# Optimization experiments

Measured on AMD Instinct MI355X. Metric: run time of the kernel, lower is better.

The kernel has to match this reference:

```python
import jax, jax.numpy as jnp
import numpy as np

# gen_dx_bx([-30,30,0.15], [-15,15,0.15])
DX = jnp.array([0.15, 0.15], dtype=jnp.float32)
BX = jnp.array([-29.925, -14.925], dtype=jnp.float32)


def _pairwise_dist(a, b):
    # torch.cdist p=2: [Na,2] x [Nb,2] -> [Na,Nb]
    return jnp.sqrt(jnp.sum((a[:, None, :] - b[None, :, :]) ** 2, axis=-1))


def _single(match, position, semantic, pts, ins, typ):
    # match [M,M] (M=N+1 with dustbin), position [N,2], semantic [C,N],
    # pts [G,2], ins [G] int, typ [G] int. Assumes mask is all-ones (set in setup_inputs).
    N = position.shape[0]
    M = match.shape[0]
    G = pts.shape[0]
    C = semantic.shape[0]

    pos = position * DX + BX                      # grid -> meters
    cd = _pairwise_dist(pos, pts)                 # [N,G]
    nearest = cd.argmin(-1).astype(jnp.int32)     # [N]
    cdist_mean = jnp.mean(cd.min(-1))             # mean of per-pred nearest-GT distance
    dist_map = _pairwise_dist(pos, pos)           # [N,N]
    nmax = nearest.max()

    # precompute, for every gt index g, whether any pred maps to it and the
    # closest such pred (torch: idx_pred_next[cdist[idx_pred_next, g].argmin()])
    assign = nearest[:, None] == jnp.arange(G, dtype=jnp.int32)[None, :]  # [N,G]
    exists_g = assign.any(0)                                              # [G]
    best_pred_g = jnp.where(assign, cd, jnp.inf).argmin(0).astype(jnp.int32)  # [G]

    def walk(start_gt):
        # greedy forward walk along gt indices; replicates the python while-loop,
        # including torch's negative-index wrap (idx % G) for idx_gt_next = -1.
        def cond(st):
            return ~st[2]

        def body(st):
            idx, steps, done, res = st
            is_end = idx >= nmax
            g_next_raw = jnp.where(is_end, jnp.int32(-1), idx + 1)
            g_next = jnp.mod(g_next_raw, G)
            ex = (~is_end) & exists_g[g_next]  # nearest==-1 never holds in torch
            same = ins[jnp.mod(idx, G)] == ins[g_next]
            matched = ex & same
            stop = matched | (~same) | (steps >= G + 2)  # safety bound
            res_new = jnp.where(matched, best_pred_g[g_next], jnp.int32(-1))
            return (g_next_raw, steps + jnp.int32(1), stop, res_new)

        st = (start_gt, jnp.int32(0), jnp.bool_(False), jnp.int32(-1))
        return jax.lax.while_loop(cond, body, st)[3]

    next_pred = jax.vmap(walk)(nearest)  # [N], -1 means no match (dustbin later)

    # build match_gt [M,M]
    A = jnp.zeros((M, M), dtype=match.dtype)
    valid = next_pred >= 0
    cols = jnp.where(valid, next_pred, 0)
    A = A.at[jnp.arange(N), cols].max(valid.astype(match.dtype))

    # resolve columns matched by multiple rows: keep the row closest in dist_map
    Acols = A[:, :N]
    col_sum = Acols.sum(0)
    dist_pad = jnp.concatenate([dist_map, jnp.full((1, N), jnp.inf, dist_map.dtype)], 0)  # [M,N]
    keep = jnp.where(Acols > 0, dist_pad, jnp.inf).argmin(0)  # [N]
    onehot = (jnp.arange(M)[:, None] == keep[None, :]).astype(match.dtype)
    Acols = jnp.where(col_sum[None, :] > 1, onehot, Acols)
    A = A.at[:, :N].set(Acols)

    # unmatched pred rows -> dustbin column; unmatched pred cols -> dustbin row
    row_sum = A[:N].sum(1)
    A = A.at[:N, M - 1].set(jnp.where(row_sum == 0, 1.0, A[:N, M - 1]))
    col_sum2 = A[:, :N].sum(0)
    A = A.at[M - 1, :N].set(jnp.where(col_sum2 == 0, 1.0, A[M - 1, :N]))

    # semantic gt: one-hot of the type of each pred's nearest gt point
    cls = typ[nearest]  # [N]
    semantic_gt = (jnp.arange(C)[:, None] == cls[None, :]).astype(semantic.dtype)  # [C,N]

    # NLL match loss (torch transposes then feeds NLLLoss: loss = -match[j, target[j]])
    tgt_b = A.argmax(0)  # per-column gt row
    tgt_f = A.argmax(1)  # per-row gt col
    j = jnp.arange(M - 1)
    loss_b = -jnp.mean(match[j, tgt_b[: M - 1]])
    loss_f = -jnp.mean(match[j, tgt_f[: M - 1]])
    match_loss = 0.5 * (loss_f + loss_b)

    sem_loss = -jnp.mean(semantic[semantic_gt.argmax(0), jnp.arange(N)])
    return cdist_mean, match_loss, sem_loss, A, semantic_gt


def setup_inputs() -> dict:
    key = jax.random.key(0)
    ks = jax.random.split(key, 5)
    B, N, G, C, NI = 4, 2048, 1024, 3, 32
    # log-probability score matrix with dustbin (Sinkhorn-style output)
    matches = jax.nn.log_softmax(jax.random.normal(ks[0], (B, N + 1, N + 1), jnp.float32), axis=-1)
    # predicted vertex grid coords on the 400x200 BEV grid
    positions = jax.random.uniform(ks[1], (B, N, 2), jnp.float32) * jnp.array([400.0, 200.0], jnp.float32)
    semantics = jax.nn.log_softmax(jax.random.normal(ks[2], (B, C, N), jnp.float32), axis=1)
    masks = jnp.ones((B, N, 1), jnp.float32)
    # gt points in meters within the BEV range
    gt_pts = (jax.random.uniform(ks[3], (B, G, 2), jnp.float32) - 0.5) * jnp.array([60.0, 30.0], jnp.float32)
    # sorted instance ids -> contiguous runs like the original per-instance list build
    gt_ins = jnp.sort(jax.random.randint(ks[4], (B, G), 0, NI), axis=-1).astype(jnp.int32)
    gt_type = (gt_ins % C).astype(jnp.int32)
    return {"matches": matches, "positions": positions, "semantics": semantics,
            "masks": masks, "gt_pts": gt_pts, "gt_ins": gt_ins, "gt_type": gt_type}


def reference(matches, positions, semantics, masks, gt_pts, gt_ins, gt_type):
    cm, ml, sl, mg, sg = jax.vmap(_single)(matches, positions, semantics, gt_pts, gt_ins, gt_type)
    # reduction='mean'
    return jnp.mean(cm), jnp.mean(ml), jnp.mean(sl), mg, sg
```

## Files before the change

### kernel.cpp

```cpp
#include <hip/hip_runtime.h>
#include <math.h>

#define BB 4
#define NN 2048
#define GG 1024
#define CC 3
#define MM 2049
#define SP 8
#define CH (GG / SP)

typedef unsigned long long u64;
#define KEY_EMPTY 0xFFFFFFFFFFFFFFFFULL

struct Ws {
  u64   near_key[BB * NN];
  u64   best_key[BB * GG];
  u64   keep_key[BB * NN];
  int   nearest[BB * NN];
  int   next_pred[BB * NN];
  int   col_cnt[BB * NN];
  int   nmax[BB];
  float cdist_sum[BB];
  float sem_sum[BB];
  float lossf_sum[BB];
  float lossb_sum[BB];
};

__device__ __forceinline__ float posx(float p) { return __fadd_rn(__fmul_rn(p, 0.15f), -29.925f); }
__device__ __forceinline__ float posy(float p) { return __fadd_rn(__fmul_rn(p, 0.15f), -14.925f); }
__device__ __forceinline__ float pdist(float ax, float ay, float bx, float by) {
  float dx = __fsub_rn(ax, bx);
  float dy = __fsub_rn(ay, by);
  return __fsqrt_rn(__fadd_rn(__fmul_rn(dx, dx), __fmul_rn(dy, dy)));
}
__device__ __forceinline__ u64 pack_key(float d, int i) {
  return ((u64)__float_as_uint(d) << 32) | (unsigned int)i;
}


__global__ void k_init(Ws* ws) {
  int t = blockIdx.x * blockDim.x + threadIdx.x;
  if (t < BB * NN) {
    ws->near_key[t] = KEY_EMPTY;
    ws->keep_key[t] = KEY_EMPTY;
    ws->col_cnt[t] = 0;
  }
  if (t < BB * GG) ws->best_key[t] = KEY_EMPTY;
  if (t < BB) {
    ws->nmax[t] = 0;
    ws->cdist_sum[t] = 0.f;
    ws->sem_sum[t] = 0.f;
    ws->lossf_sum[t] = 0.f;
    ws->lossb_sum[t] = 0.f;
  }
}

__global__ __launch_bounds__(256) void k_near1(const float* __restrict__ positions,
                                               const float* __restrict__ gt_pts, Ws* ws) {
  __shared__ float spts[CH * 2];
  const int cpb = NN / 256;
  int b = blockIdx.x / (cpb * SP);
  int r = blockIdx.x % (cpb * SP);
  int i = (r / SP) * 256 + threadIdx.x;
  int g0 = (r % SP) * CH;

  spts[threadIdx.x] = gt_pts[b * GG * 2 + g0 * 2 + threadIdx.x];
  __syncthreads();

  float px = posx(positions[(size_t)(b * NN + i) * 2 + 0]);
  float py = posy(positions[(size_t)(b * NN + i) * 2 + 1]);

  float dmin = INFINITY;
  int gmin = 0;
  #pragma unroll 4
  for (int g = 0; g < CH; ++g) {
    float d = pdist(px, py, spts[2 * g], spts[2 * g + 1]);
    if (d < dmin) { dmin = d; gmin = g; }
  }
  atomicMin(&ws->near_key[b * NN + i], pack_key(dmin, g0 + gmin));
}

__global__ __launch_bounds__(64) void k_near2(const int* __restrict__ gt_type,
                                              const float* __restrict__ semantics,
                                              Ws* ws, float* __restrict__ out) {
  int b = blockIdx.x >> 5;
  int i = (blockIdx.x & 31) * 64 + threadIdx.x;

  u64 key = ws->near_key[b * NN + i];
  float dmin = __uint_as_float((unsigned int)(key >> 32));
  int g = (int)(key & 0xFFFFFFFFULL);

  ws->nearest[b * NN + i] = g;
  atomicMin(&ws->best_key[b * GG + g], pack_key(dmin, i));

  int cls = gt_type[b * GG + g];
  float* sg = out + 3 + (size_t)BB * MM * MM;
  sg[(size_t)b * CC * NN + 0 * NN + i] = (cls == 0) ? 1.f : 0.f;
  sg[(size_t)b * CC * NN + 1 * NN + i] = (cls == 1) ? 1.f : 0.f;
  sg[(size_t)b * CC * NN + 2 * NN + i] = (cls == 2) ? 1.f : 0.f;
  float sem = semantics[(size_t)b * CC * NN + (size_t)cls * NN + i];

  float v = dmin;
  #pragma unroll
  for (int o = 32; o > 0; o >>= 1) v += __shfl_down(v, o, 64);
  if (threadIdx.x == 0) atomicAdd(&ws->cdist_sum[b], v);

  v = sem;
  #pragma unroll
  for (int o = 32; o > 0; o >>= 1) v += __shfl_down(v, o, 64);
  if (threadIdx.x == 0) atomicAdd(&ws->sem_sum[b], v);

  int m = g;
  #pragma unroll
  for (int o = 32; o > 0; o >>= 1) m = max(m, __shfl_down(m, o, 64));
  if (threadIdx.x == 0) atomicMax(&ws->nmax[b], m);
}

__global__ __launch_bounds__(64) void k_walk(const int* __restrict__ gt_ins,
                                             const float* __restrict__ positions, Ws* ws) {
  __shared__ int sins[GG];
  __shared__ int sbest[GG];
  int b = blockIdx.x >> 5;
  int i = (blockIdx.x & 31) * 64 + threadIdx.x;

  {
    const int4* src = reinterpret_cast<const int4*>(gt_ins + b * GG);
    int4* dst = reinterpret_cast<int4*>(sins);
    for (int t = threadIdx.x; t < GG / 4; t += 64) dst[t] = src[t];
    const u64* bk = ws->best_key + b * GG;
    for (int t = threadIdx.x; t < GG; t += 64) {
      u64 k = bk[t];
      sbest[t] = (k == KEY_EMPTY) ? -1 : (int)(k & 0xFFFFFFFFULL);
    }
  }
  __syncthreads();

  int nmax = ws->nmax[b];
  int idx = ws->nearest[b * NN + i];
  int steps = 0, res = -1;
  while (true) {
    bool is_end = idx >= nmax;
    int gnr = is_end ? -1 : idx + 1;
    int gn = gnr & (GG - 1);
    bool ex = (!is_end) && (sbest[gn] >= 0);
    bool same = sins[idx & (GG - 1)] == sins[gn];
    bool matched = ex && same;
    res = matched ? sbest[gn] : -1;
    bool stop = matched || (!same) || (steps >= GG + 2);
    idx = gnr;
    ++steps;
    if (stop) break;
  }
  ws->next_pred[b * NN + i] = res;
  if (res >= 0) {
    atomicAdd(&ws->col_cnt[b * NN + res], 1);
    const float* pb = positions + (size_t)b * NN * 2;
    float d = pdist(posx(pb[2 * i]), posy(pb[2 * i + 1]),
                    posx(pb[2 * res]), posy(pb[2 * res + 1]));
    atomicMin(&ws->keep_key[b * NN + res], pack_key(d, i));
  }
}

__global__ __launch_bounds__(64) void k_post(const float* __restrict__ matches,
                                             Ws* ws, float* __restrict__ out) {
  int b = blockIdx.x >> 5;
  int i = (blockIdx.x & 31) * 64 + threadIdx.x;

  float* A = out + 3 + (size_t)b * MM * MM;

  int j = ws->next_pred[b * NN + i];
  bool surv = (j >= 0) && ((int)(ws->keep_key[b * NN + j] & 0xFFFFFFFFULL) == i);
  if (surv) A[(size_t)i * MM + j] = 1.0f;
  else      A[(size_t)i * MM + (MM - 1)] = 1.0f;

  int cnt = ws->col_cnt[b * NN + i];
  if (cnt == 0) A[(size_t)(MM - 1) * MM + i] = 1.0f;

  int tf = surv ? j : (MM - 1);
  float vf = matches[(size_t)b * MM * MM + (size_t)i * MM + tf];
  int tb = (cnt > 0) ? (int)(ws->keep_key[b * NN + i] & 0xFFFFFFFFULL) : (MM - 1);
  float vb = matches[(size_t)b * MM * MM + (size_t)i * MM + tb];

  float v = vf;
  #pragma unroll
  for (int o = 32; o > 0; o >>= 1) v += __shfl_down(v, o, 64);
  if (threadIdx.x == 0) atomicAdd(&ws->lossf_sum[b], v);

  v = vb;
  #pragma unroll
  for (int o = 32; o > 0; o >>= 1) v += __shfl_down(v, o, 64);
  if (threadIdx.x == 0) atomicAdd(&ws->lossb_sum[b], v);
}

__global__ void k_final(Ws* ws, float* __restrict__ out) {
  if (threadIdx.x == 0 && blockIdx.x == 0) {
    float cm = 0.f, ml = 0.f, sl = 0.f;
    for (int b = 0; b < BB; ++b) {
      cm += ws->cdist_sum[b] / (float)NN;
      float lf = -(ws->lossf_sum[b] / (float)(MM - 1));
      float lb = -(ws->lossb_sum[b] / (float)(MM - 1));
      ml += 0.5f * (lf + lb);
      sl += -(ws->sem_sum[b] / (float)NN);
    }
    out[0] = cm / (float)BB;
    out[1] = ml / (float)BB;
    out[2] = sl / (float)BB;
  }
}

extern "C" void kernel_launch(void* const* d_in, const int* in_sizes, int n_in,
                              void* d_out, int out_size, void* d_ws, size_t ws_size,
                              hipStream_t stream) {
  (void)in_sizes; (void)n_in; (void)ws_size;
  const float* matches   = (const float*)d_in[0];
  const float* positions = (const float*)d_in[1];
  const float* semantics = (const float*)d_in[2];
  const float* gt_pts    = (const float*)d_in[4];
  const int*   gt_ins    = (const int*)d_in[5];
  const int*   gt_type   = (const int*)d_in[6];
  float* out = (float*)d_out;
  Ws* ws = (Ws*)d_ws;

  hipMemsetAsync(d_out, 0, (size_t)out_size * sizeof(float), stream);
  k_init<<<(BB * NN + 255) / 256, 256, 0, stream>>>(ws);
  k_near1<<<BB * (NN / 256) * SP, 256, 0, stream>>>(positions, gt_pts, ws);
  k_near2<<<BB * (NN / 64), 64, 0, stream>>>(gt_type, semantics, ws, out);
  k_walk<<<BB * (NN / 64), 64, 0, stream>>>(gt_ins, positions, ws);
  k_post<<<BB * (NN / 64), 64, 0, stream>>>(matches, ws, out);
  k_final<<<1, 64, 0, stream>>>(ws, out);
}
```

Baseline: 150.8 us.

## Fuse nearest-search, walk and post kernels; fold output zeroing into kernel

Replaces the six-step launch sequence with three kernels. The nearest-GT search now splits each point's 1024 GT candidates across 8 lanes and reduces packed keys with shuffles instead of global atomics. The walk and post phases are fused into one 1024-thread block per batch that keeps counts and keep-keys in shared memory. The large output memset is replaced by a grid-stride float4 zeroing inside k_near, which removes the separate memset and init kernels. The cost is that the walk/post phase now runs on only 4 blocks, so most of the GPU sits idle during it.

```diff
diff --git a/kernel.cpp b/kernel.cpp
--- a/kernel.cpp
+++ b/kernel.cpp
@@ -6,22 +6,20 @@
 #define GG 1024
 #define CC 3
 #define MM 2049
-#define SP 8
-#define CH (GG / SP)
+#define ABEG 3
+#define ASZ (BB * MM * MM)
+#define AEND (ABEG + ASZ)
+#define A4BEG 4
+#define NF4 ((AEND - A4BEG) / 4)
 
 typedef unsigned long long u64;
 #define KEY_EMPTY 0xFFFFFFFFFFFFFFFFULL
 
 struct Ws {
-  u64   near_key[BB * NN];
   u64   best_key[BB * GG];
-  u64   keep_key[BB * NN];
   int   nearest[BB * NN];
-  int   next_pred[BB * NN];
-  int   col_cnt[BB * NN];
-  int   nmax[BB];
-  float cdist_sum[BB];
-  float sem_sum[BB];
+  float cdist_part[256];
+  float sem_part[256];
   float lossf_sum[BB];
   float lossb_sum[BB];
 };
@@ -37,170 +35,197 @@
   return ((u64)__float_as_uint(d) << 32) | (unsigned int)i;
 }
 
-
-__global__ void k_init(Ws* ws) {
-  int t = blockIdx.x * blockDim.x + threadIdx.x;
-  if (t < BB * NN) {
-    ws->near_key[t] = KEY_EMPTY;
-    ws->keep_key[t] = KEY_EMPTY;
-    ws->col_cnt[t] = 0;
-  }
-  if (t < BB * GG) ws->best_key[t] = KEY_EMPTY;
-  if (t < BB) {
-    ws->nmax[t] = 0;
-    ws->cdist_sum[t] = 0.f;
-    ws->sem_sum[t] = 0.f;
-    ws->lossf_sum[t] = 0.f;
-    ws->lossb_sum[t] = 0.f;
-  }
-}
-
-__global__ __launch_bounds__(256) void k_near1(const float* __restrict__ positions,
-                                               const float* __restrict__ gt_pts, Ws* ws) {
-  __shared__ float spts[CH * 2];
-  const int cpb = NN / 256;
-  int b = blockIdx.x / (cpb * SP);
-  int r = blockIdx.x % (cpb * SP);
-  int i = (r / SP) * 256 + threadIdx.x;
-  int g0 = (r % SP) * CH;
-
-  spts[threadIdx.x] = gt_pts[b * GG * 2 + g0 * 2 + threadIdx.x];
-  __syncthreads();
-
-  float px = posx(positions[(size_t)(b * NN + i) * 2 + 0]);
-  float py = posy(positions[(size_t)(b * NN + i) * 2 + 1]);
-
-  float dmin = INFINITY;
-  int gmin = 0;
-  #pragma unroll 4
-  for (int g = 0; g < CH; ++g) {
-    float d = pdist(px, py, spts[2 * g], spts[2 * g + 1]);
-    if (d < dmin) { dmin = d; gmin = g; }
-  }
-  atomicMin(&ws->near_key[b * NN + i], pack_key(dmin, g0 + gmin));
-}
-
-__global__ __launch_bounds__(64) void k_near2(const int* __restrict__ gt_type,
+__global__ __launch_bounds__(256) void k_near(const float* __restrict__ positions,
+                                              const float* __restrict__ gt_pts,
+                                              const int* __restrict__ gt_type,
                                               const float* __restrict__ semantics,
                                               Ws* ws, float* __restrict__ out) {
-  int b = blockIdx.x >> 5;
-  int i = (blockIdx.x & 31) * 64 + threadIdx.x;
-
-  u64 key = ws->near_key[b * NN + i];
-  float dmin = __uint_as_float((unsigned int)(key >> 32));
-  int g = (int)(key & 0xFFFFFFFFULL);
-
-  ws->nearest[b * NN + i] = g;
-  atomicMin(&ws->best_key[b * GG + g], pack_key(dmin, i));
-
-  int cls = gt_type[b * GG + g];
-  float* sg = out + 3 + (size_t)BB * MM * MM;
-  sg[(size_t)b * CC * NN + 0 * NN + i] = (cls == 0) ? 1.f : 0.f;
-  sg[(size_t)b * CC * NN + 1 * NN + i] = (cls == 1) ? 1.f : 0.f;
-  sg[(size_t)b * CC * NN + 2 * NN + i] = (cls == 2) ? 1.f : 0.f;
-  float sem = semantics[(size_t)b * CC * NN + (size_t)cls * NN + i];
-
-  float v = dmin;
-  #pragma unroll
-  for (int o = 32; o > 0; o >>= 1) v += __shfl_down(v, o, 64);
-  if (threadIdx.x == 0) atomicAdd(&ws->cdist_sum[b], v);
-
-  v = sem;
-  #pragma unroll
-  for (int o = 32; o > 0; o >>= 1) v += __shfl_down(v, o, 64);
-  if (threadIdx.x == 0) atomicAdd(&ws->sem_sum[b], v);
-
-  int m = g;
-  #pragma unroll
-  for (int o = 32; o > 0; o >>= 1) m = max(m, __shfl_down(m, o, 64));
-  if (threadIdx.x == 0) atomicMax(&ws->nmax[b], m);
-}
-
-__global__ __launch_bounds__(64) void k_walk(const int* __restrict__ gt_ins,
-                                             const float* __restrict__ positions, Ws* ws) {
-  __shared__ int sins[GG];
-  __shared__ int sbest[GG];
-  int b = blockIdx.x >> 5;
-  int i = (blockIdx.x & 31) * 64 + threadIdx.x;
+  __shared__ float spts[GG * 2];
+  __shared__ float sdm[32], ssm[32];
+  const int bid = blockIdx.x, tid = threadIdx.x;
+  const int b = bid >> 6, blk = bid & 63;
+  const int p = tid >> 3, q = tid & 7;
+  const int i = blk * 32 + p;
 
   {
-    const int4* src = reinterpret_cast<const int4*>(gt_ins + b * GG);
-    int4* dst = reinterpret_cast<int4*>(sins);
-    for (int t = threadIdx.x; t < GG / 4; t += 64) dst[t] = src[t];
-    const u64* bk = ws->best_key + b * GG;
-    for (int t = threadIdx.x; t < GG; t += 64) {
-      u64 k = bk[t];
-      sbest[t] = (k == KEY_EMPTY) ? -1 : (int)(k & 0xFFFFFFFFULL);
-    }
-  }
-  __syncthreads();
-
-  int nmax = ws->nmax[b];
-  int idx = ws->nearest[b * NN + i];
-  int steps = 0, res = -1;
-  while (true) {
-    bool is_end = idx >= nmax;
-    int gnr = is_end ? -1 : idx + 1;
-    int gn = gnr & (GG - 1);
-    bool ex = (!is_end) && (sbest[gn] >= 0);
-    bool same = sins[idx & (GG - 1)] == sins[gn];
-    bool matched = ex && same;
-    res = matched ? sbest[gn] : -1;
-    bool stop = matched || (!same) || (steps >= GG + 2);
-    idx = gnr;
-    ++steps;
-    if (stop) break;
-  }
-  ws->next_pred[b * NN + i] = res;
-  if (res >= 0) {
-    atomicAdd(&ws->col_cnt[b * NN + res], 1);
-    const float* pb = positions + (size_t)b * NN * 2;
-    float d = pdist(posx(pb[2 * i]), posy(pb[2 * i + 1]),
-                    posx(pb[2 * res]), posy(pb[2 * res + 1]));
-    atomicMin(&ws->keep_key[b * NN + res], pack_key(d, i));
-  }
-}
-
-__global__ __launch_bounds__(64) void k_post(const float* __restrict__ matches,
-                                             Ws* ws, float* __restrict__ out) {
-  int b = blockIdx.x >> 5;
-  int i = (blockIdx.x & 31) * 64 + threadIdx.x;
-
-  float* A = out + 3 + (size_t)b * MM * MM;
-
-  int j = ws->next_pred[b * NN + i];
-  bool surv = (j >= 0) && ((int)(ws->keep_key[b * NN + j] & 0xFFFFFFFFULL) == i);
-  if (surv) A[(size_t)i * MM + j] = 1.0f;
-  else      A[(size_t)i * MM + (MM - 1)] = 1.0f;
-
-  int cnt = ws->col_cnt[b * NN + i];
-  if (cnt == 0) A[(size_t)(MM - 1) * MM + i] = 1.0f;
-
-  int tf = surv ? j : (MM - 1);
-  float vf = matches[(size_t)b * MM * MM + (size_t)i * MM + tf];
-  int tb = (cnt > 0) ? (int)(ws->keep_key[b * NN + i] & 0xFFFFFFFFULL) : (MM - 1);
-  float vb = matches[(size_t)b * MM * MM + (size_t)i * MM + tb];
-
-  float v = vf;
-  #pragma unroll
-  for (int o = 32; o > 0; o >>= 1) v += __shfl_down(v, o, 64);
-  if (threadIdx.x == 0) atomicAdd(&ws->lossf_sum[b], v);
-
-  v = vb;
-  #pragma unroll
-  for (int o = 32; o > 0; o >>= 1) v += __shfl_down(v, o, 64);
-  if (threadIdx.x == 0) atomicAdd(&ws->lossb_sum[b], v);
-}
-
-__global__ void k_final(Ws* ws, float* __restrict__ out) {
-  if (threadIdx.x == 0 && blockIdx.x == 0) {
+    const float4* src = reinterpret_cast<const float4*>(gt_pts + b * GG * 2);
+    float4* dst = reinterpret_cast<float4*>(spts);
+    dst[tid] = src[tid];
+    dst[tid + 256] = src[tid + 256];
+  }
+  {
+    float4 z = make_float4(0.f, 0.f, 0.f, 0.f);
+    float4* o4 = reinterpret_cast<float4*>(out + A4BEG);
+    int gt = bid * 256 + tid;
+    for (int t = gt; t < NF4; t += 256 * 256) o4[t] = z;
+    if (gt == 3) out[ABEG] = 0.f;
+    if (gt < 3) out[AEND - 3 + gt] = 0.f;
+  }
+  __syncthreads();
+
+  float2 pp = reinterpret_cast<const float2*>(positions)[b * NN + i];
+  float px = posx(pp.x), py = posy(pp.y);
+
+  u64 key = KEY_EMPTY;
+  const int g0 = q * 128;
+  #pragma unroll 4
+  for (int k = 0; k < 128; ++k) {
+    int o = (k + 2 * q) & 127;
+    int g = g0 + o;
+    float d = pdist(px, py, spts[2 * g], spts[2 * g + 1]);
+    u64 kk = pack_key(d, g);
+    key = kk < key ? kk : key;
+  }
+  #pragma unroll
+  for (int m = 4; m > 0; m >>= 1) {
+    u64 other = __shfl_xor(key, m, 64);
+    key = other < key ? other : key;
+  }
+
+  if (q == 0) {
+    float dmin = __uint_as_float((unsigned int)(key >> 32));
+    int g = (int)(key & 0xFFFFFFFFULL);
+    ws->nearest[b * NN + i] = g;
+    atomicMin(&ws->best_key[b * GG + g], pack_key(dmin, i));
+
+    int cls = gt_type[b * GG + g];
+    float* sg = out + AEND;
+    sg[(size_t)b * CC * NN + 0 * NN + i] = (cls == 0) ? 1.f : 0.f;
+    sg[(size_t)b * CC * NN + 1 * NN + i] = (cls == 1) ? 1.f : 0.f;
+    sg[(size_t)b * CC * NN + 2 * NN + i] = (cls == 2) ? 1.f : 0.f;
+    sdm[p] = dmin;
+    ssm[p] = semantics[(size_t)b * CC * NN + (size_t)cls * NN + i];
+  }
+  __syncthreads();
+  if (tid < 32) {
+    float v1 = sdm[tid], v2 = ssm[tid];
+    #pragma unroll
+    for (int o = 16; o > 0; o >>= 1) {
+      v1 += __shfl_down(v1, o, 32);
+      v2 += __shfl_down(v2, o, 32);
+    }
+    if (tid == 0) { ws->cdist_part[bid] = v1; ws->sem_part[bid] = v2; }
+  }
+}
+
+__global__ __launch_bounds__(1024) void k_walkpost(const int* __restrict__ gt_ins,
+                                                   const float* __restrict__ positions,
+                                                   const float* __restrict__ matches,
+                                                   Ws* ws, float* __restrict__ out) {
+  __shared__ int   sins[GG];
+  __shared__ int   sbest[GG];
+  __shared__ int   scnt[NN];
+  __shared__ u64   skeep[NN];
+  __shared__ int   snmax[16];
+  __shared__ float swf[16], swb[16];
+  const int b = blockIdx.x, tid = threadIdx.x;
+  const int wv = tid >> 6, ln = tid & 63;
+
+  if (tid < GG / 4)
+    reinterpret_cast<int4*>(sins)[tid] = reinterpret_cast<const int4*>(gt_ins + b * GG)[tid];
+  int cand;
+  {
+    u64 k = ws->best_key[b * GG + tid];
+    int v = (k == KEY_EMPTY) ? -1 : (int)(k & 0xFFFFFFFFULL);
+    sbest[tid] = v;
+    cand = (v >= 0) ? tid : 0;
+  }
+  scnt[tid] = 0;         scnt[tid + 1024] = 0;
+  skeep[tid] = KEY_EMPTY; skeep[tid + 1024] = KEY_EMPTY;
+  #pragma unroll
+  for (int o = 32; o > 0; o >>= 1) cand = max(cand, __shfl_down(cand, o, 64));
+  if (ln == 0) snmax[wv] = cand;
+  __syncthreads();
+  int nmax = snmax[0];
+  #pragma unroll
+  for (int w = 1; w < 16; ++w) nmax = max(nmax, snmax[w]);
+
+  const float* pb = positions + (size_t)b * NN * 2;
+
+  int res[2];
+  #pragma unroll
+  for (int s = 0; s < 2; ++s) {
+    int i = tid + s * 1024;
+    int idx = ws->nearest[b * NN + i];
+    int steps = 0, r = -1;
+    while (true) {
+      bool is_end = idx >= nmax;
+      int gnr = is_end ? -1 : idx + 1;
+      int gn = gnr & (GG - 1);
+      bool ex = (!is_end) && (sbest[gn] >= 0);
+      bool same = sins[idx & (GG - 1)] == sins[gn];
+      bool matched = ex && same;
+      r = matched ? sbest[gn] : -1;
+      bool stop = matched || (!same) || (steps >= GG + 2);
+      idx = gnr;
+      ++steps;
+      if (stop) break;
+    }
+    res[s] = r;
+    if (r >= 0) {
+      atomicAdd(&scnt[r], 1);
+      float2 pi = reinterpret_cast<const float2*>(pb)[i];
+      float2 pr = reinterpret_cast<const float2*>(pb)[r];
+      float d = pdist(posx(pi.x), posy(pi.y), posx(pr.x), posy(pr.y));
+      atomicMin(&skeep[r], pack_key(d, i));
+    }
+  }
+  __syncthreads();
+
+  float* A = out + ABEG + (size_t)b * MM * MM;
+  const float* mb = matches + (size_t)b * MM * MM;
+  float accf = 0.f, accb = 0.f;
+  #pragma unroll
+  for (int s = 0; s < 2; ++s) {
+    int i = tid + s * 1024;
+    int j = res[s];
+    bool surv = (j >= 0) && ((int)(skeep[j] & 0xFFFFFFFFULL) == i);
+    if (surv) A[(size_t)i * MM + j] = 1.0f;
+    else      A[(size_t)i * MM + (MM - 1)] = 1.0f;
+    int cnt = scnt[i];
+    if (cnt == 0) A[(size_t)(MM - 1) * MM + i] = 1.0f;
+    int tf = surv ? j : (MM - 1);
+    accf += mb[(size_t)i * MM + tf];
+    int tb = (cnt > 0) ? (int)(skeep[i] & 0xFFFFFFFFULL) : (MM - 1);
+    accb += mb[(size_t)i * MM + tb];
+  }
+  #pragma unroll
+  for (int o = 32; o > 0; o >>= 1) {
+    accf += __shfl_down(accf, o, 64);
+    accb += __shfl_down(accb, o, 64);
+  }
+  if (ln == 0) { swf[wv] = accf; swb[wv] = accb; }
+  __syncthreads();
+  if (tid == 0) {
+    float sf = 0.f, sb = 0.f;
+    #pragma unroll
+    for (int w = 0; w < 16; ++w) { sf += swf[w]; sb += swb[w]; }
+    ws->lossf_sum[b] = sf;
+    ws->lossb_sum[b] = sb;
+  }
+}
+
+__global__ __launch_bounds__(256) void k_final(Ws* ws, float* __restrict__ out) {
+  __shared__ float scd[4], ssm2[4];
+  const int tid = threadIdx.x;
+  const int w = tid >> 6, ln = tid & 63;
+  float v1 = ws->cdist_part[w * 64 + ln];
+  float v2 = ws->sem_part[w * 64 + ln];
+  #pragma unroll
+  for (int o = 32; o > 0; o >>= 1) {
+    v1 += __shfl_down(v1, o, 64);
+    v2 += __shfl_down(v2, o, 64);
+  }
+  if (ln == 0) { scd[w] = v1; ssm2[w] = v2; }
+  __syncthreads();
+  if (tid == 0) {
     float cm = 0.f, ml = 0.f, sl = 0.f;
     for (int b = 0; b < BB; ++b) {
-      cm += ws->cdist_sum[b] / (float)NN;
+      cm += scd[b] / (float)NN;
       float lf = -(ws->lossf_sum[b] / (float)(MM - 1));
       float lb = -(ws->lossb_sum[b] / (float)(MM - 1));
       ml += 0.5f * (lf + lb);
-      sl += -(ws->sem_sum[b] / (float)NN);
+      sl += -(ssm2[b] / (float)NN);
     }
     out[0] = cm / (float)BB;
     out[1] = ml / (float)BB;
@@ -211,7 +236,7 @@
 extern "C" void kernel_launch(void* const* d_in, const int* in_sizes, int n_in,
                               void* d_out, int out_size, void* d_ws, size_t ws_size,
                               hipStream_t stream) {
-  (void)in_sizes; (void)n_in; (void)ws_size;
+  (void)in_sizes; (void)n_in; (void)ws_size; (void)out_size;
   const float* matches   = (const float*)d_in[0];
   const float* positions = (const float*)d_in[1];
   const float* semantics = (const float*)d_in[2];
@@ -221,11 +246,8 @@
   float* out = (float*)d_out;
   Ws* ws = (Ws*)d_ws;
 
-  hipMemsetAsync(d_out, 0, (size_t)out_size * sizeof(float), stream);
-  k_init<<<(BB * NN + 255) / 256, 256, 0, stream>>>(ws);
-  k_near1<<<BB * (NN / 256) * SP, 256, 0, stream>>>(positions, gt_pts, ws);
-  k_near2<<<BB * (NN / 64), 64, 0, stream>>>(gt_type, semantics, ws, out);
-  k_walk<<<BB * (NN / 64), 64, 0, stream>>>(gt_ins, positions, ws);
-  k_post<<<BB * (NN / 64), 64, 0, stream>>>(matches, ws, out);
-  k_final<<<1, 64, 0, stream>>>(ws, out);
-}
+  hipMemsetAsync(ws, 0xFF, sizeof(u64) * BB * GG, stream);
+  k_near<<<BB * 64, 256, 0, stream>>>(positions, gt_pts, gt_type, semantics, ws, out);
+  k_walkpost<<<BB, 1024, 0, stream>>>(gt_ins, positions, matches, ws, out);
+  k_final<<<1, 256, 0, stream>>>(ws, out);
+}
```

After: 145.4 us. -3.5%, faster.
